# Kernel tuning notes

Measured on AMD Instinct MI355X. Metric: run time of the kernel, lower is better.

Reference implementation:

```python
import jax, jax.numpy as jnp
import numpy as np


def setup_inputs() -> dict:
    key = jax.random.key(0)
    k1, k2 = jax.random.split(key)
    B, S, D, L = 4, 4096, 256, 8921
    x = jax.random.normal(k1, (B, S, D), dtype=jnp.float32)
    U = jax.random.normal(k2, (L, D), dtype=jnp.float32)
    return {"x": x, "U": U}


def reference(x, U):
    # scores: [B, L, S] = U [L,D] @ x^T [B,D,S]
    scores = jnp.einsum('ld,bsd->bls', U, x)
    # softmax over seq dim (dim=2 in torch)
    alpha = jax.nn.softmax(scores, axis=2)
    # pooled: [B, L, D]
    out = jnp.einsum('bls,bsd->bld', alpha, x)
    return (out, alpha)
```

## Files before the change

kernel.cpp:

```cpp
#include <hip/hip_runtime.h>

#define B_DIM 4
#define S_DIM 4096
#define D_DIM 256
#define L_DIM 8921

typedef _Float16 f16x8 __attribute__((ext_vector_type(8)));
typedef _Float16 f16x4 __attribute__((ext_vector_type(4)));
typedef float    f32x4 __attribute__((ext_vector_type(4)));

__global__ __launch_bounds__(256) void k_split_x(const float* __restrict__ x,
                                                 _Float16* __restrict__ xh,
                                                 _Float16* __restrict__ xl) {
  const size_t i = ((size_t)blockIdx.x * 256 + threadIdx.x) * 4;
  float4 v = *(const float4*)(x + i);
  f16x4 h, l;
  h.x = (_Float16)v.x; l.x = (_Float16)(v.x - (float)h.x);
  h.y = (_Float16)v.y; l.y = (_Float16)(v.y - (float)h.y);
  h.z = (_Float16)v.z; l.z = (_Float16)(v.z - (float)h.z);
  h.w = (_Float16)v.w; l.w = (_Float16)(v.w - (float)h.w);
  *(f16x4*)(xh + i) = h;
  *(f16x4*)(xl + i) = l;
}

__global__ __launch_bounds__(256) void k_split_u(const float* __restrict__ U,
                                                 _Float16* __restrict__ uh,
                                                 _Float16* __restrict__ ul) {
  const size_t i = ((size_t)blockIdx.x * 256 + threadIdx.x) * 4;
  if (i >= (size_t)L_DIM * D_DIM) return;
  float4 v = *(const float4*)(U + i);
  f16x4 h, l;
  h.x = (_Float16)v.x; l.x = (_Float16)(v.x - (float)h.x);
  h.y = (_Float16)v.y; l.y = (_Float16)(v.y - (float)h.y);
  h.z = (_Float16)v.z; l.z = (_Float16)(v.z - (float)h.z);
  h.w = (_Float16)v.w; l.w = (_Float16)(v.w - (float)h.w);
  *(f16x4*)(uh + i) = h;
  *(f16x4*)(ul + i) = l;
}

__global__ __launch_bounds__(256) void k_transpose(const float* __restrict__ x,
                                                   _Float16* __restrict__ xT) {
  __shared__ _Float16 t[32][33];
  const int s0 = blockIdx.x * 32, d0 = blockIdx.y * 32, b = blockIdx.z;
  const float* xb = x + (size_t)b * S_DIM * D_DIM;
  const int r = threadIdx.x >> 5, c = threadIdx.x & 31;
#pragma unroll
  for (int p = 0; p < 4; ++p) {
    const int row = r + p * 8;
    t[row][c] = (_Float16)xb[(size_t)(s0 + row) * D_DIM + d0 + c];
  }
  __syncthreads();
  _Float16* xtb = xT + (size_t)b * D_DIM * S_DIM;
#pragma unroll
  for (int p = 0; p < 4; ++p) {
    const int row = r + p * 8;
    xtb[(size_t)(d0 + row) * S_DIM + s0 + c] = t[c][row];
  }
}

__global__ __launch_bounds__(256) void k_scores(const _Float16* __restrict__ Uh,
                                                const _Float16* __restrict__ Ul,
                                                const _Float16* __restrict__ Xh,
                                                const _Float16* __restrict__ Xl,
                                                float* __restrict__ scores) {
  const int s0 = blockIdx.x * 128;
  const int l0 = blockIdx.y * 128;
  const int b  = blockIdx.z;

  __shared__ _Float16 Ah[128 * 32], Al[128 * 32], Bh[128 * 32], Bl[128 * 32];

  const int tid = threadIdx.x;
  const int wave = tid >> 6, lane = tid & 63;
  const int wm = wave & 1, wn = wave >> 1;

  const _Float16* Xbh = Xh + (size_t)b * S_DIM * D_DIM;
  const _Float16* Xbl = Xl + (size_t)b * S_DIM * D_DIM;

  f32x4 acc[4][4] = {};

  const int srow = tid >> 2;
  const int soff = (tid & 3) * 8;

  for (int k0 = 0; k0 < D_DIM; k0 += 32) {
#pragma unroll
    for (int p = 0; p < 2; ++p) {
      const int row = srow + p * 64;
      const int l = l0 + row;
      uint4 vh = make_uint4(0, 0, 0, 0), vl = make_uint4(0, 0, 0, 0);
      if (l < L_DIM) {
        vh = *(const uint4*)(Uh + (size_t)l * D_DIM + k0 + soff);
        vl = *(const uint4*)(Ul + (size_t)l * D_DIM + k0 + soff);
      }
      *(uint4*)(Ah + row * 32 + soff) = vh;
      *(uint4*)(Al + row * 32 + soff) = vl;
      const int s = s0 + row;
      *(uint4*)(Bh + row * 32 + soff) =
          *(const uint4*)(Xbh + (size_t)s * D_DIM + k0 + soff);
      *(uint4*)(Bl + row * 32 + soff) =
          *(const uint4*)(Xbl + (size_t)s * D_DIM + k0 + soff);
    }
    __syncthreads();

    const int frow = lane & 15;
    const int fk = (lane >> 4) * 8;
    f16x8 ah[4], al[4], bh[4], bl[4];
#pragma unroll
    for (int i = 0; i < 4; ++i) {
      ah[i] = *(const f16x8*)(Ah + (wm * 64 + i * 16 + frow) * 32 + fk);
      al[i] = *(const f16x8*)(Al + (wm * 64 + i * 16 + frow) * 32 + fk);
      bh[i] = *(const f16x8*)(Bh + (wn * 64 + i * 16 + frow) * 32 + fk);
      bl[i] = *(const f16x8*)(Bl + (wn * 64 + i * 16 + frow) * 32 + fk);
    }
#pragma unroll
    for (int i = 0; i < 4; ++i)
#pragma unroll
      for (int j = 0; j < 4; ++j) {
        acc[i][j] = __builtin_amdgcn_mfma_f32_16x16x32_f16(ah[i], bh[j], acc[i][j], 0, 0, 0);
        acc[i][j] = __builtin_amdgcn_mfma_f32_16x16x32_f16(ah[i], bl[j], acc[i][j], 0, 0, 0);
        acc[i][j] = __builtin_amdgcn_mfma_f32_16x16x32_f16(al[i], bh[j], acc[i][j], 0, 0, 0);
      }
    __syncthreads();
  }

  float* sc = scores + (size_t)b * L_DIM * S_DIM;
#pragma unroll
  for (int i = 0; i < 4; ++i)
#pragma unroll
    for (int j = 0; j < 4; ++j) {
      const int col = s0 + wn * 64 + j * 16 + (lane & 15);
#pragma unroll
      for (int r = 0; r < 4; ++r) {
        const int row = l0 + wm * 64 + i * 16 + (lane >> 4) * 4 + r;
        if (row < L_DIM) sc[(size_t)row * S_DIM + col] = acc[i][j][r];
      }
    }
}

__global__ __launch_bounds__(256) void k_stats(const float* __restrict__ scores,
                                               float* __restrict__ stats) {
  const int l = blockIdx.x;
  const int b = blockIdx.y;
  const float* row = scores + ((size_t)b * L_DIM + l) * S_DIM;
  const int tid = threadIdx.x;
  const float4* rp = (const float4*)(row + tid * 16);
  const float4 a0 = rp[0], a1 = rp[1], a2 = rp[2], a3 = rp[3];

  float m = fmaxf(fmaxf(fmaxf(a0.x, a0.y), fmaxf(a0.z, a0.w)),
                  fmaxf(fmaxf(fmaxf(a1.x, a1.y), fmaxf(a1.z, a1.w)),
                        fmaxf(fmaxf(fmaxf(a2.x, a2.y), fmaxf(a2.z, a2.w)),
                              fmaxf(fmaxf(a3.x, a3.y), fmaxf(a3.z, a3.w)))));
#pragma unroll
  for (int off = 32; off >= 1; off >>= 1) m = fmaxf(m, __shfl_xor(m, off));

  __shared__ float redm[4], reds[4];
  const int wave = tid >> 6, lane = tid & 63;
  if (lane == 0) redm[wave] = m;
  __syncthreads();
  m = fmaxf(fmaxf(redm[0], redm[1]), fmaxf(redm[2], redm[3]));

  float s = __expf(a0.x - m) + __expf(a0.y - m) + __expf(a0.z - m) + __expf(a0.w - m)
          + __expf(a1.x - m) + __expf(a1.y - m) + __expf(a1.z - m) + __expf(a1.w - m)
          + __expf(a2.x - m) + __expf(a2.y - m) + __expf(a2.z - m) + __expf(a2.w - m)
          + __expf(a3.x - m) + __expf(a3.y - m) + __expf(a3.z - m) + __expf(a3.w - m);
#pragma unroll
  for (int off = 32; off >= 1; off >>= 1) s += __shfl_xor(s, off);
  if (lane == 0) reds[wave] = s;
  __syncthreads();
  if (tid == 0) {
    const float tot = reds[0] + reds[1] + reds[2] + reds[3];
    float* st = stats + ((size_t)b * L_DIM + l) * 2;
    st[0] = m;
    st[1] = 1.0f / tot;
  }
}

__global__ __launch_bounds__(256) void k_out(const _Float16* __restrict__ XT,
                                             const float* __restrict__ stats,
                                             float* __restrict__ alpha,
                                             float* __restrict__ out) {
  const int l0 = blockIdx.x * 64;
  const int b  = blockIdx.y;
  const int tid = threadIdx.x;
  const int wave = tid >> 6, lane = tid & 63;

  __shared__ _Float16 Aa[64 * 32];
  __shared__ _Float16 Bb[256 * 32];
  __shared__ float sm[64], sr[64];

  if (tid < 64) {
    const int l = l0 + tid;
    float m = 0.f, r = 0.f;
    if (l < L_DIM) {
      const float* st = stats + ((size_t)b * L_DIM + l) * 2;
      m = st[0];
      r = st[1];
    }
    sm[tid] = m;
    sr[tid] = r;
  }
  __syncthreads();

  f32x4 acc[4][4] = {};
  float* al_base = alpha + (size_t)b * L_DIM * S_DIM;
  const _Float16* xt = XT + (size_t)b * D_DIM * S_DIM;

  const int arow = tid >> 3, aoff = (tid & 7) * 4;
  const int brow = tid >> 2, boff = (tid & 3) * 8;

  for (int s0 = 0; s0 < S_DIM; s0 += 32) {
#pragma unroll
    for (int p = 0; p < 2; ++p) {
      const int row = arow + p * 32;
      const int l = l0 + row;
      float4 v = make_float4(0.f, 0.f, 0.f, 0.f);
      if (l < L_DIM) {
        float* ap = al_base + (size_t)l * S_DIM + s0 + aoff;
        v = *(const float4*)ap;
        const float m = sm[row], r = sr[row];
        v.x = __expf(v.x - m) * r;
        v.y = __expf(v.y - m) * r;
        v.z = __expf(v.z - m) * r;
        v.w = __expf(v.w - m) * r;
        *(float4*)ap = v;
      }
      f16x4 pk;
      pk.x = (_Float16)v.x;
      pk.y = (_Float16)v.y;
      pk.z = (_Float16)v.z;
      pk.w = (_Float16)v.w;
      *(f16x4*)(Aa + row * 32 + aoff) = pk;
    }
#pragma unroll
    for (int p = 0; p < 4; ++p) {
      const int row = brow + p * 64;
      *(uint4*)(Bb + row * 32 + boff) =
          *(const uint4*)(xt + (size_t)row * S_DIM + s0 + boff);
    }
    __syncthreads();

    const int frow = lane & 15;
    const int fk = (lane >> 4) * 8;
    f16x8 af[4], bf[4];
#pragma unroll
    for (int i = 0; i < 4; ++i) {
      af[i] = *(const f16x8*)(Aa + (i * 16 + frow) * 32 + fk);
      bf[i] = *(const f16x8*)(Bb + (wave * 64 + i * 16 + frow) * 32 + fk);
    }
#pragma unroll
    for (int i = 0; i < 4; ++i)
#pragma unroll
      for (int j = 0; j < 4; ++j)
        acc[i][j] = __builtin_amdgcn_mfma_f32_16x16x32_f16(af[i], bf[j], acc[i][j], 0, 0, 0);
    __syncthreads();
  }

  float* ob = out + (size_t)b * L_DIM * D_DIM;
#pragma unroll
  for (int i = 0; i < 4; ++i)
#pragma unroll
    for (int j = 0; j < 4; ++j) {
      const int d = wave * 64 + j * 16 + (lane & 15);
#pragma unroll
      for (int r = 0; r < 4; ++r) {
        const int l = l0 + i * 16 + (lane >> 4) * 4 + r;
        if (l < L_DIM) ob[(size_t)l * D_DIM + d] = acc[i][j][r];
      }
    }
}

extern "C" void kernel_launch(void* const* d_in, const int* in_sizes, int n_in,
                              void* d_out, int out_size, void* d_ws, size_t ws_size,
                              hipStream_t stream) {
  const float* x = (const float*)d_in[0];
  const float* U = (const float*)d_in[1];
  float* out   = (float*)d_out;
  float* alpha = out + (size_t)B_DIM * L_DIM * D_DIM;

  const size_t NX = (size_t)B_DIM * S_DIM * D_DIM;
  const size_t NU = (size_t)L_DIM * D_DIM;

  char* w = (char*)d_ws;
  _Float16* xh = (_Float16*)w; w += NX * 2;
  _Float16* xl = (_Float16*)w; w += NX * 2;
  _Float16* xT = (_Float16*)w; w += NX * 2;
  _Float16* uh = (_Float16*)w; w += NU * 2;
  _Float16* ul = (_Float16*)w; w += NU * 2;
  float* stats = (float*)w;

  k_split_x<<<dim3((unsigned)(NX / 1024)), 256, 0, stream>>>(x, xh, xl);
  k_split_u<<<dim3((unsigned)((NU / 4 + 255) / 256)), 256, 0, stream>>>(U, uh, ul);
  k_transpose<<<dim3(S_DIM / 32, D_DIM / 32, B_DIM), 256, 0, stream>>>(x, xT);
  k_scores<<<dim3(S_DIM / 128, (L_DIM + 127) / 128, B_DIM), 256, 0, stream>>>(
      uh, ul, xh, xl, alpha);
  k_stats<<<dim3(L_DIM, B_DIM), 256, 0, stream>>>(alpha, stats);
  k_out<<<dim3((L_DIM + 63) / 64, B_DIM), 256, 0, stream>>>(xT, stats, alpha, out);
}
```

Before: 1.307 ms.

## Fuse softmax row stats into score GEMM epilogue and use async LDS loads

The scores GEMM now computes per-tile row max and sum-of-exp in its epilogue and writes partials, which a small reduce kernel merges. This replaces the separate stats pass that re-read the full scores matrix. The GEMM also loads tiles with global_load_lds and an XOR swizzle, with U padded to L_PAD so loads need no bounds checks. k_out moves to 32-row tiles with padded LDS rows, giving more blocks and fewer bank conflicts at the cost of less B-tile reuse.

```diff
diff --git a/kernel.cpp b/kernel.cpp
--- a/kernel.cpp
+++ b/kernel.cpp
@@ -4,10 +4,17 @@
 #define S_DIM 4096
 #define D_DIM 256
 #define L_DIM 8921
+#define L_PAD 8960
 
 typedef _Float16 f16x8 __attribute__((ext_vector_type(8)));
 typedef _Float16 f16x4 __attribute__((ext_vector_type(4)));
 typedef float    f32x4 __attribute__((ext_vector_type(4)));
+
+__device__ __forceinline__ void cp16(_Float16* lds, const _Float16* g) {
+  __builtin_amdgcn_global_load_lds(
+      (const __attribute__((address_space(1))) unsigned int*)g,
+      (__attribute__((address_space(3))) unsigned int*)lds, 16, 0, 0);
+}
 
 __global__ __launch_bounds__(256) void k_split_x(const float* __restrict__ x,
                                                  _Float16* __restrict__ xh,
@@ -27,8 +34,9 @@
                                                  _Float16* __restrict__ uh,
                                                  _Float16* __restrict__ ul) {
   const size_t i = ((size_t)blockIdx.x * 256 + threadIdx.x) * 4;
-  if (i >= (size_t)L_DIM * D_DIM) return;
-  float4 v = *(const float4*)(U + i);
+  if (i >= (size_t)L_PAD * D_DIM) return;
+  float4 v = make_float4(0.f, 0.f, 0.f, 0.f);
+  if (i < (size_t)L_DIM * D_DIM) v = *(const float4*)(U + i);
   f16x4 h, l;
   h.x = (_Float16)v.x; l.x = (_Float16)(v.x - (float)h.x);
   h.y = (_Float16)v.y; l.y = (_Float16)(v.y - (float)h.y);
@@ -62,12 +70,16 @@
                                                 const _Float16* __restrict__ Ul,
                                                 const _Float16* __restrict__ Xh,
                                                 const _Float16* __restrict__ Xl,
-                                                float* __restrict__ scores) {
+                                                float* __restrict__ scores,
+                                                float2* __restrict__ part) {
   const int s0 = blockIdx.x * 128;
   const int l0 = blockIdx.y * 128;
   const int b  = blockIdx.z;
 
-  __shared__ _Float16 Ah[128 * 32], Al[128 * 32], Bh[128 * 32], Bl[128 * 32];
+  __shared__ __attribute__((aligned(16))) _Float16 Ah[128 * 32];
+  __shared__ __attribute__((aligned(16))) _Float16 Al[128 * 32];
+  __shared__ __attribute__((aligned(16))) _Float16 Bh[128 * 32];
+  __shared__ __attribute__((aligned(16))) _Float16 Bl[128 * 32];
 
   const int tid = threadIdx.x;
   const int wave = tid >> 6, lane = tid & 63;
@@ -76,40 +88,40 @@
   const _Float16* Xbh = Xh + (size_t)b * S_DIM * D_DIM;
   const _Float16* Xbl = Xl + (size_t)b * S_DIM * D_DIM;
 
+  const int srow = tid >> 2;
+  const int csrc = ((tid & 3) ^ ((tid >> 3) & 3)) * 8;
+  const size_t urow0 = (size_t)(l0 + srow) * D_DIM + csrc;
+  const size_t urow1 = urow0 + (size_t)64 * D_DIM;
+  const size_t xrow0 = (size_t)(s0 + srow) * D_DIM + csrc;
+  const size_t xrow1 = xrow0 + (size_t)64 * D_DIM;
+  _Float16* d0 = (_Float16*)0 + tid * 8;
+  const int ldso = tid * 8;
+
+  const int frow = lane & 15;
+  const int ck = ((lane >> 4) ^ ((frow >> 1) & 3)) * 8;
+
   f32x4 acc[4][4] = {};
 
-  const int srow = tid >> 2;
-  const int soff = (tid & 3) * 8;
-
   for (int k0 = 0; k0 < D_DIM; k0 += 32) {
-#pragma unroll
-    for (int p = 0; p < 2; ++p) {
-      const int row = srow + p * 64;
-      const int l = l0 + row;
-      uint4 vh = make_uint4(0, 0, 0, 0), vl = make_uint4(0, 0, 0, 0);
-      if (l < L_DIM) {
-        vh = *(const uint4*)(Uh + (size_t)l * D_DIM + k0 + soff);
-        vl = *(const uint4*)(Ul + (size_t)l * D_DIM + k0 + soff);
-      }
-      *(uint4*)(Ah + row * 32 + soff) = vh;
-      *(uint4*)(Al + row * 32 + soff) = vl;
-      const int s = s0 + row;
-      *(uint4*)(Bh + row * 32 + soff) =
-          *(const uint4*)(Xbh + (size_t)s * D_DIM + k0 + soff);
-      *(uint4*)(Bl + row * 32 + soff) =
-          *(const uint4*)(Xbl + (size_t)s * D_DIM + k0 + soff);
-    }
+    cp16(Ah + ldso,        Uh + urow0 + k0);
+    cp16(Ah + 2048 + ldso, Uh + urow1 + k0);
+    cp16(Al + ldso,        Ul + urow0 + k0);
+    cp16(Al + 2048 + ldso, Ul + urow1 + k0);
+    cp16(Bh + ldso,        Xbh + xrow0 + k0);
+    cp16(Bh + 2048 + ldso, Xbh + xrow1 + k0);
+    cp16(Bl + ldso,        Xbl + xrow0 + k0);
+    cp16(Bl + 2048 + ldso, Xbl + xrow1 + k0);
     __syncthreads();
 
-    const int frow = lane & 15;
-    const int fk = (lane >> 4) * 8;
     f16x8 ah[4], al[4], bh[4], bl[4];
 #pragma unroll
     for (int i = 0; i < 4; ++i) {
-      ah[i] = *(const f16x8*)(Ah + (wm * 64 + i * 16 + frow) * 32 + fk);
-      al[i] = *(const f16x8*)(Al + (wm * 64 + i * 16 + frow) * 32 + fk);
-      bh[i] = *(const f16x8*)(Bh + (wn * 64 + i * 16 + frow) * 32 + fk);
-      bl[i] = *(const f16x8*)(Bl + (wn * 64 + i * 16 + frow) * 32 + fk);
+      const int ra = (wm * 64 + i * 16 + frow) * 32 + ck;
+      const int rb = (wn * 64 + i * 16 + frow) * 32 + ck;
+      ah[i] = *(const f16x8*)(Ah + ra);
+      al[i] = *(const f16x8*)(Al + ra);
+      bh[i] = *(const f16x8*)(Bh + rb);
+      bl[i] = *(const f16x8*)(Bl + rb);
     }
 #pragma unroll
     for (int i = 0; i < 4; ++i)
@@ -121,8 +133,10 @@
       }
     __syncthreads();
   }
+  (void)d0;
 
   float* sc = scores + (size_t)b * L_DIM * S_DIM;
+  const int hi = lane >> 4;
 #pragma unroll
   for (int i = 0; i < 4; ++i)
 #pragma unroll
@@ -130,64 +144,83 @@
       const int col = s0 + wn * 64 + j * 16 + (lane & 15);
 #pragma unroll
       for (int r = 0; r < 4; ++r) {
-        const int row = l0 + wm * 64 + i * 16 + (lane >> 4) * 4 + r;
+        const int row = l0 + wm * 64 + i * 16 + hi * 4 + r;
         if (row < L_DIM) sc[(size_t)row * S_DIM + col] = acc[i][j][r];
       }
     }
-}
-
-__global__ __launch_bounds__(256) void k_stats(const float* __restrict__ scores,
-                                               float* __restrict__ stats) {
-  const int l = blockIdx.x;
-  const int b = blockIdx.y;
-  const float* row = scores + ((size_t)b * L_DIM + l) * S_DIM;
-  const int tid = threadIdx.x;
-  const float4* rp = (const float4*)(row + tid * 16);
-  const float4 a0 = rp[0], a1 = rp[1], a2 = rp[2], a3 = rp[3];
-
-  float m = fmaxf(fmaxf(fmaxf(a0.x, a0.y), fmaxf(a0.z, a0.w)),
-                  fmaxf(fmaxf(fmaxf(a1.x, a1.y), fmaxf(a1.z, a1.w)),
-                        fmaxf(fmaxf(fmaxf(a2.x, a2.y), fmaxf(a2.z, a2.w)),
-                              fmaxf(fmaxf(a3.x, a3.y), fmaxf(a3.z, a3.w)))));
-#pragma unroll
-  for (int off = 32; off >= 1; off >>= 1) m = fmaxf(m, __shfl_xor(m, off));
-
-  __shared__ float redm[4], reds[4];
-  const int wave = tid >> 6, lane = tid & 63;
-  if (lane == 0) redm[wave] = m;
+
+  float* redm = (float*)Ah;
+  float* reds = redm + 256;
+#pragma unroll
+  for (int i = 0; i < 4; ++i)
+#pragma unroll
+    for (int r = 0; r < 4; ++r) {
+      float m = fmaxf(fmaxf(acc[i][0][r], acc[i][1][r]),
+                      fmaxf(acc[i][2][r], acc[i][3][r]));
+      m = fmaxf(m, __shfl_xor(m, 1));
+      m = fmaxf(m, __shfl_xor(m, 2));
+      m = fmaxf(m, __shfl_xor(m, 4));
+      m = fmaxf(m, __shfl_xor(m, 8));
+      float s = __expf(acc[i][0][r] - m) + __expf(acc[i][1][r] - m) +
+                __expf(acc[i][2][r] - m) + __expf(acc[i][3][r] - m);
+      s += __shfl_xor(s, 1);
+      s += __shfl_xor(s, 2);
+      s += __shfl_xor(s, 4);
+      s += __shfl_xor(s, 8);
+      if ((lane & 15) == 0) {
+        const int row64 = i * 16 + hi * 4 + r;
+        redm[(wm * 2 + wn) * 64 + row64] = m;
+        reds[(wm * 2 + wn) * 64 + row64] = s;
+      }
+    }
   __syncthreads();
-  m = fmaxf(fmaxf(redm[0], redm[1]), fmaxf(redm[2], redm[3]));
-
-  float s = __expf(a0.x - m) + __expf(a0.y - m) + __expf(a0.z - m) + __expf(a0.w - m)
-          + __expf(a1.x - m) + __expf(a1.y - m) + __expf(a1.z - m) + __expf(a1.w - m)
-          + __expf(a2.x - m) + __expf(a2.y - m) + __expf(a2.z - m) + __expf(a2.w - m)
-          + __expf(a3.x - m) + __expf(a3.y - m) + __expf(a3.z - m) + __expf(a3.w - m);
-#pragma unroll
-  for (int off = 32; off >= 1; off >>= 1) s += __shfl_xor(s, off);
-  if (lane == 0) reds[wave] = s;
-  __syncthreads();
-  if (tid == 0) {
-    const float tot = reds[0] + reds[1] + reds[2] + reds[3];
-    float* st = stats + ((size_t)b * L_DIM + l) * 2;
-    st[0] = m;
-    st[1] = 1.0f / tot;
-  }
+  if (tid < 128) {
+    const int wmm = tid >> 6, r64 = tid & 63;
+    const float m0 = redm[(wmm * 2 + 0) * 64 + r64];
+    const float m1 = redm[(wmm * 2 + 1) * 64 + r64];
+    const float s0v = reds[(wmm * 2 + 0) * 64 + r64];
+    const float s1v = reds[(wmm * 2 + 1) * 64 + r64];
+    const float m = fmaxf(m0, m1);
+    const float s = s0v * __expf(m0 - m) + s1v * __expf(m1 - m);
+    const int l = l0 + tid;
+    if (l < L_DIM)
+      part[((size_t)blockIdx.x * B_DIM + b) * L_PAD + l] = make_float2(m, s);
+  }
+}
+
+__global__ __launch_bounds__(256) void k_sreduce(const float2* __restrict__ part,
+                                                 float* __restrict__ stats) {
+  const int idx = blockIdx.x * 256 + threadIdx.x;
+  if (idx >= B_DIM * L_DIM) return;
+  const int b = idx / L_DIM;
+  const int l = idx - b * L_DIM;
+  float2 v[32];
+#pragma unroll
+  for (int t = 0; t < 32; ++t) v[t] = part[((size_t)t * B_DIM + b) * L_PAD + l];
+  float m = v[0].x;
+#pragma unroll
+  for (int t = 1; t < 32; ++t) m = fmaxf(m, v[t].x);
+  float s = 0.f;
+#pragma unroll
+  for (int t = 0; t < 32; ++t) s += v[t].y * __expf(v[t].x - m);
+  stats[2 * (size_t)idx]     = m;
+  stats[2 * (size_t)idx + 1] = 1.0f / s;
 }
 
 __global__ __launch_bounds__(256) void k_out(const _Float16* __restrict__ XT,
                                              const float* __restrict__ stats,
                                              float* __restrict__ alpha,
                                              float* __restrict__ out) {
-  const int l0 = blockIdx.x * 64;
+  const int l0 = blockIdx.x * 32;
   const int b  = blockIdx.y;
   const int tid = threadIdx.x;
   const int wave = tid >> 6, lane = tid & 63;
 
-  __shared__ _Float16 Aa[64 * 32];
-  __shared__ _Float16 Bb[256 * 32];
-  __shared__ float sm[64], sr[64];
-
-  if (tid < 64) {
+  __shared__ __attribute__((aligned(16))) _Float16 Aa[32 * 40];
+  __shared__ __attribute__((aligned(16))) _Float16 Bb[256 * 40];
+  __shared__ float sm[32], sr[32];
+
+  if (tid < 32) {
     const int l = l0 + tid;
     float m = 0.f, r = 0.f;
     if (l < L_DIM) {
@@ -200,54 +233,49 @@
   }
   __syncthreads();
 
-  f32x4 acc[4][4] = {};
+  f32x4 acc[2][4] = {};
   float* al_base = alpha + (size_t)b * L_DIM * S_DIM;
   const _Float16* xt = XT + (size_t)b * D_DIM * S_DIM;
 
   const int arow = tid >> 3, aoff = (tid & 7) * 4;
   const int brow = tid >> 2, boff = (tid & 3) * 8;
+  const float m_r = sm[arow], r_r = sr[arow];
+  const int l_a = l0 + arow;
+  const int frow = lane & 15, fk = (lane >> 4) * 8;
 
   for (int s0 = 0; s0 < S_DIM; s0 += 32) {
-#pragma unroll
-    for (int p = 0; p < 2; ++p) {
-      const int row = arow + p * 32;
-      const int l = l0 + row;
-      float4 v = make_float4(0.f, 0.f, 0.f, 0.f);
-      if (l < L_DIM) {
-        float* ap = al_base + (size_t)l * S_DIM + s0 + aoff;
-        v = *(const float4*)ap;
-        const float m = sm[row], r = sr[row];
-        v.x = __expf(v.x - m) * r;
-        v.y = __expf(v.y - m) * r;
-        v.z = __expf(v.z - m) * r;
-        v.w = __expf(v.w - m) * r;
-        *(float4*)ap = v;
-      }
-      f16x4 pk;
-      pk.x = (_Float16)v.x;
-      pk.y = (_Float16)v.y;
-      pk.z = (_Float16)v.z;
-      pk.w = (_Float16)v.w;
-      *(f16x4*)(Aa + row * 32 + aoff) = pk;
-    }
+    float4 v = make_float4(0.f, 0.f, 0.f, 0.f);
+    if (l_a < L_DIM) {
+      float* ap = al_base + (size_t)l_a * S_DIM + s0 + aoff;
+      v = *(const float4*)ap;
+      v.x = __expf(v.x - m_r) * r_r;
+      v.y = __expf(v.y - m_r) * r_r;
+      v.z = __expf(v.z - m_r) * r_r;
+      v.w = __expf(v.w - m_r) * r_r;
+      *(float4*)ap = v;
+    }
+    f16x4 pk;
+    pk.x = (_Float16)v.x;
+    pk.y = (_Float16)v.y;
+    pk.z = (_Float16)v.z;
+    pk.w = (_Float16)v.w;
+    *(f16x4*)(Aa + arow * 40 + aoff) = pk;
 #pragma unroll
     for (int p = 0; p < 4; ++p) {
       const int row = brow + p * 64;
-      *(uint4*)(Bb + row * 32 + boff) =
+      *(uint4*)(Bb + row * 40 + boff) =
           *(const uint4*)(xt + (size_t)row * S_DIM + s0 + boff);
     }
     __syncthreads();
 
-    const int frow = lane & 15;
-    const int fk = (lane >> 4) * 8;
-    f16x8 af[4], bf[4];
-#pragma unroll
-    for (int i = 0; i < 4; ++i) {
-      af[i] = *(const f16x8*)(Aa + (i * 16 + frow) * 32 + fk);
-      bf[i] = *(const f16x8*)(Bb + (wave * 64 + i * 16 + frow) * 32 + fk);
-    }
-#pragma unroll
-    for (int i = 0; i < 4; ++i)
+    f16x8 af[2], bf[4];
+    af[0] = *(const f16x8*)(Aa + frow * 40 + fk);
+    af[1] = *(const f16x8*)(Aa + (16 + frow) * 40 + fk);
+#pragma unroll
+    for (int j = 0; j < 4; ++j)
+      bf[j] = *(const f16x8*)(Bb + (wave * 64 + j * 16 + frow) * 40 + fk);
+#pragma unroll
+    for (int i = 0; i < 2; ++i)
 #pragma unroll
       for (int j = 0; j < 4; ++j)
         acc[i][j] = __builtin_amdgcn_mfma_f32_16x16x32_f16(af[i], bf[j], acc[i][j], 0, 0, 0);
@@ -256,7 +284,7 @@
 
   float* ob = out + (size_t)b * L_DIM * D_DIM;
 #pragma unroll
-  for (int i = 0; i < 4; ++i)
+  for (int i = 0; i < 2; ++i)
 #pragma unroll
     for (int j = 0; j < 4; ++j) {
       const int d = wave * 64 + j * 16 + (lane & 15);
@@ -276,22 +304,23 @@
   float* out   = (float*)d_out;
   float* alpha = out + (size_t)B_DIM * L_DIM * D_DIM;
 
-  const size_t NX = (size_t)B_DIM * S_DIM * D_DIM;
-  const size_t NU = (size_t)L_DIM * D_DIM;
+  const size_t NX  = (size_t)B_DIM * S_DIM * D_DIM;
+  const size_t NUP = (size_t)L_PAD * D_DIM;
 
   char* w = (char*)d_ws;
   _Float16* xh = (_Float16*)w; w += NX * 2;
   _Float16* xl = (_Float16*)w; w += NX * 2;
   _Float16* xT = (_Float16*)w; w += NX * 2;
-  _Float16* uh = (_Float16*)w; w += NU * 2;
-  _Float16* ul = (_Float16*)w; w += NU * 2;
-  float* stats = (float*)w;
+  _Float16* uh = (_Float16*)w; w += NUP * 2;
+  _Float16* ul = (_Float16*)w; w += NUP * 2;
+  float* stats = (float*)w;    w += (size_t)B_DIM * L_DIM * 2 * sizeof(float);
+  float2* part = (float2*)w;
 
   k_split_x<<<dim3((unsigned)(NX / 1024)), 256, 0, stream>>>(x, xh, xl);
-  k_split_u<<<dim3((unsigned)((NU / 4 + 255) / 256)), 256, 0, stream>>>(U, uh, ul);
+  k_split_u<<<dim3((unsigned)(NUP / 1024)), 256, 0, stream>>>(U, uh, ul);
   k_transpose<<<dim3(S_DIM / 32, D_DIM / 32, B_DIM), 256, 0, stream>>>(x, xT);
-  k_scores<<<dim3(S_DIM / 128, (L_DIM + 127) / 128, B_DIM), 256, 0, stream>>>(
-      uh, ul, xh, xl, alpha);
-  k_stats<<<dim3(L_DIM, B_DIM), 256, 0, stream>>>(alpha, stats);
-  k_out<<<dim3((L_DIM + 63) / 64, B_DIM), 256, 0, stream>>>(xT, stats, alpha, out);
-}
+  k_scores<<<dim3(S_DIM / 128, L_PAD / 128, B_DIM), 256, 0, stream>>>(
+      uh, ul, xh, xl, alpha, part);
+  k_sreduce<<<dim3((B_DIM * L_DIM + 255) / 256), 256, 0, stream>>>(part, stats);
+  k_out<<<dim3((L_DIM + 31) / 32, B_DIM), 256, 0, stream>>>(xT, stats, alpha, out);
+}
```

Measured after the change: 1.323 ms. About the same (+1.2%).
